# Optimization experiments

Hardware: AMD Instinct MI355X
Metric: run time of the kernel (lower is better)

Reference implementation:

```python
import jax, jax.numpy as jnp
import numpy as np

H = 16          # num_attention_heads
D = 64          # attention_head_size
HID = H * D     # hidden_size
FF = 4096       # intermediate_size
W = 128         # attention_half_width
EPS = 1e-8


def setup_inputs() -> dict:
    key = jax.random.key(0)
    ks = jax.random.split(key, 16)
    s = 0.02
    return {
        "hidden_states": jax.random.normal(ks[0], (1, 2048, HID), jnp.float32),
        "attention_mask": jnp.ones((1, 2048), dtype=bool),
        # projections stored as [in, out] (transposed torch Linear weight)
        "wq": jax.random.normal(ks[1], (HID, HID), jnp.float32) * s,
        "wk": jax.random.normal(ks[2], (HID, HID), jnp.float32) * s,
        "wv": jax.random.normal(ks[3], (HID, HID), jnp.float32) * s,
        "pos_key": jax.random.normal(ks[4], (H, D, 2 * W + 1), jnp.float32),
        "pos_query": jax.random.normal(ks[5], (H, D, 2 * W + 1), jnp.float32),
        "wo": jax.random.normal(ks[6], (HID, HID), jnp.float32) * s,
        "bo": jnp.zeros((HID,), jnp.float32),
        "ln1_g": jnp.ones((HID,), jnp.float32),
        "ln1_b": jnp.zeros((HID,), jnp.float32),
        "ln2_g": jnp.ones((HID,), jnp.float32),
        "ln2_b": jnp.zeros((HID,), jnp.float32),
        "w1": jax.random.normal(ks[7], (HID, FF), jnp.float32) * s,
        "b1": jnp.zeros((FF,), jnp.float32),
        "w2": jax.random.normal(ks[8], (FF, HID), jnp.float32) * s,
        "b2": jnp.zeros((HID,), jnp.float32),
    }


def _layer_norm(x, g, b):
    mu = jnp.mean(x, axis=-1, keepdims=True)
    var = jnp.mean(jnp.square(x - mu), axis=-1, keepdims=True)
    return (x - mu) * jax.lax.rsqrt(var + EPS) * g + b


def _encoder_layer(hidden_states, attention_mask, wq, wk, wv, pos_key,
                   pos_query, wo, bo, ln1_g, ln1_b, ln2_g, ln2_b, w1, b1, w2, b2):
    B, L, _ = hidden_states.shape
    m = attention_mask  # [B, L] bool

    # --- local self-attention with disentangled relative bias ---
    x1 = _layer_norm(hidden_states, ln1_g, ln1_b)
    q = (x1 @ wq).reshape(B, L, H, D).transpose(0, 2, 1, 3)  # [B,H,L,D]
    k = (x1 @ wk).reshape(B, L, H, D).transpose(0, 2, 1, 3)
    v = (x1 @ wv).reshape(B, L, H, D).transpose(0, 2, 1, 3)

    score = jnp.einsum('bhqd,bhkd->bhqk', q, k)  # [B,H,L,L]

    # relative position index: idx[i,j] = clip(w - (i-j), 0, 2w)
    ids = jnp.arange(L)
    idx = jnp.clip(W - (ids[:, None] - ids[None, :]), 0, 2 * W)  # [L,L]
    idx_b = jnp.broadcast_to(idx[None, None], (B, H, L, L))

    c2p = jnp.einsum('bhld,hdp->bhlp', q, pos_key)     # [B,H,L,2w+1]
    score_c2p = jnp.take_along_axis(c2p, idx_b, axis=-1)
    p2c = jnp.einsum('bhld,hdp->bhlp', k, pos_query)
    score_p2c = jnp.take_along_axis(p2c, idx_b, axis=-1).swapaxes(-1, -2)
    score = score + score_c2p + score_p2c

    band = jnp.abs(ids[:, None] - ids[None, :]) <= W   # [L,L]
    em = band[None, None] & m[:, None, None, :] & m[:, None, :, None]
    lv = jnp.finfo(score.dtype).min
    score = jnp.where(em, score, lv)
    proba = jax.nn.softmax(score, axis=-1)

    ctx = jnp.einsum('bhqk,bhkd->bhqd', proba, v)
    ctx = ctx.transpose(0, 2, 1, 3).reshape(B, L, HID)
    attn_out = ctx @ wo + bo
    h = hidden_states + attn_out  # NoGating residual

    # --- feedforward ---
    x2 = _layer_norm(h, ln2_g, ln2_b)
    ff = jax.nn.gelu(x2 @ w1 + b1, approximate=False) @ w2 + b2
    return h + ff


def reference(hidden_states, attention_mask, wq, wk, wv, pos_key, pos_query,
              wo, bo, ln1_g, ln1_b, ln2_g, ln2_b, w1, b1, w2, b2):
    return _encoder_layer(hidden_states, attention_mask, wq, wk, wv, pos_key,
                          pos_query, wo, bo, ln1_g, ln1_b, ln2_g, ln2_b,
                          w1, b1, w2, b2)
```

## Files before the change

kernel.cpp:

```cpp
#include <hip/hip_runtime.h>
#include <hip/hip_bf16.h>
#include <cstdint>

typedef __hip_bfloat16 bf16;
typedef __attribute__((ext_vector_type(8))) short short8;
typedef __attribute__((ext_vector_type(4))) float f32x4;
typedef __attribute__((address_space(1))) const unsigned int gu32;
typedef __attribute__((address_space(3))) unsigned int lu32;

#define L_SEQ 2048
#define HID_  1024
#define NH    16
#define HD    64
#define FF_   4096
#define NPOS  257
#define WHALF 128
#define QKVS  3072
#define NTILE 32
#define BT_TILE (320 * 64)

__device__ inline float b2f(bf16 v) { return __bfloat162float(v); }
__device__ inline short f2bs(float f) {
    bf16 b = __float2bfloat16(f);
    return *reinterpret_cast<short*>(&b);
}

__global__ __launch_bounds__(256) void k_transpose_tiled(const float* __restrict__ src,
                                                         bf16* __restrict__ dst,
                                                         int K, int N) {
    const int k0 = blockIdx.x * 64, n0 = blockIdx.y * 64;
    __shared__ float t[64][65];
    const int c = threadIdx.x & 63, r4 = threadIdx.x >> 6;
    #pragma unroll
    for (int i = 0; i < 16; ++i)
        t[i * 4 + r4][c] = src[(size_t)(k0 + i * 4 + r4) * N + n0 + c];
    __syncthreads();
    #pragma unroll
    for (int i = 0; i < 16; ++i) {
        int n = i * 4 + r4;
        dst[(size_t)(n0 + n) * K + k0 + c] = __float2bfloat16(t[c][n]);
    }
}

__global__ void k_pos_transpose(const float* __restrict__ src, bf16* __restrict__ dst) {
    const int total = NH * NPOS * HD;
    for (int idx = blockIdx.x * blockDim.x + threadIdx.x; idx < total;
         idx += gridDim.x * blockDim.x) {
        int d = idx & 63;
        int r = idx >> 6;
        int t = r % NPOS;
        int h = r / NPOS;
        dst[idx] = __float2bfloat16(src[((size_t)h * HD + d) * NPOS + t]);
    }
}

__global__ __launch_bounds__(256) void k_layernorm(const float* __restrict__ x,
                                                   const float* __restrict__ g,
                                                   const float* __restrict__ b,
                                                   bf16* __restrict__ out) {
    const int row = blockIdx.x, tid = threadIdx.x;
    const int lane = tid & 63, w = tid >> 6;
    const float4 v = *(const float4*)(x + (size_t)row * HID_ + tid * 4);
    float vals[4] = {v.x, v.y, v.z, v.w};
    float s = vals[0] + vals[1] + vals[2] + vals[3];
    float ss = vals[0]*vals[0] + vals[1]*vals[1] + vals[2]*vals[2] + vals[3]*vals[3];
    for (int off = 32; off; off >>= 1) { s += __shfl_down(s, off); ss += __shfl_down(ss, off); }
    __shared__ float rs[4], rss[4], mv[2];
    if (lane == 0) { rs[w] = s; rss[w] = ss; }
    __syncthreads();
    if (tid == 0) {
        float S = rs[0] + rs[1] + rs[2] + rs[3];
        float SS = rss[0] + rss[1] + rss[2] + rss[3];
        float mean = S * (1.0f / HID_);
        float var = SS * (1.0f / HID_) - mean * mean;
        mv[0] = mean; mv[1] = rsqrtf(var + 1e-8f);
    }
    __syncthreads();
    const float mean = mv[0], rstd = mv[1];
    #pragma unroll
    for (int e = 0; e < 4; ++e) {
        int c = tid * 4 + e;
        out[(size_t)row * HID_ + c] = __float2bfloat16((vals[e] - mean) * rstd * g[c] + b[c]);
    }
}

template <int EPI>
__global__ __launch_bounds__(256) void k_gemm64(const bf16* __restrict__ A,
                                                const bf16* __restrict__ B,
                                                bf16* __restrict__ outB,
                                                float* __restrict__ outF,
                                                const float* __restrict__ bias,
                                                int N, int K, int kTiles, int MN) {
    __shared__ __align__(16) short As[2][2048];
    __shared__ __align__(16) short Bs[2][4096];
    const int tid = threadIdx.x;
    const int bm = blockIdx.x * 64, bn = blockIdx.y * 128;
    const int lane = tid & 63, w = tid >> 6;
    const int wr = w >> 1, wc = w & 1;
    const int k0base = blockIdx.z * kTiles * 32;

    const int crow = lane >> 2;
    const int c16p = lane & 3;
    const int coll = (c16p ^ (crow & 3)) * 8;
    const short* Ag = (const short*)A;
    const short* Bg = (const short*)B;
    const size_t a_off = (size_t)(bm + w * 16 + crow) * K + coll;
    const size_t b_off0 = (size_t)(bn + w * 32 + crow) * K + coll;
    const size_t b_off1 = (size_t)(bn + w * 32 + 16 + crow) * K + coll;

    auto stage = [&](int buf, int k0) {
        __builtin_amdgcn_global_load_lds((gu32*)(Ag + a_off + k0), (lu32*)&As[buf][w * 512], 16, 0, 0);
        __builtin_amdgcn_global_load_lds((gu32*)(Bg + b_off0 + k0), (lu32*)&Bs[buf][w * 1024], 16, 0, 0);
        __builtin_amdgcn_global_load_lds((gu32*)(Bg + b_off1 + k0), (lu32*)&Bs[buf][w * 1024 + 512], 16, 0, 0);
    };

    const int fr = lane & 15, kq = lane >> 4;
    const int xbyte = ((kq ^ (fr & 3)) << 4);

    f32x4 acc[2][4] = {};
    stage(0, k0base);
    __syncthreads();

    for (int t = 0; t < kTiles; ++t) {
        if (t + 1 < kTiles) stage((t + 1) & 1, k0base + (t + 1) * 32);
        const char* Ab = (const char*)As[t & 1];
        const char* Bb = (const char*)Bs[t & 1];
        short8 af[2], bfv[4];
        #pragma unroll
        for (int m2 = 0; m2 < 2; ++m2)
            af[m2] = *(const short8*)(Ab + ((wr * 32 + m2 * 16 + fr) << 6) + xbyte);
        #pragma unroll
        for (int n2 = 0; n2 < 4; ++n2)
            bfv[n2] = *(const short8*)(Bb + ((wc * 64 + n2 * 16 + fr) << 6) + xbyte);
        #pragma unroll
        for (int m2 = 0; m2 < 2; ++m2)
            #pragma unroll
            for (int n2 = 0; n2 < 4; ++n2)
                acc[m2][n2] = __builtin_amdgcn_mfma_f32_16x16x32_bf16(af[m2], bfv[n2], acc[m2][n2], 0, 0, 0);
        __syncthreads();
    }

    const int cr = kq * 4, cc = fr;
    #pragma unroll
    for (int m2 = 0; m2 < 2; ++m2) {
        #pragma unroll
        for (int n2 = 0; n2 < 4; ++n2) {
            const int col = bn + wc * 64 + n2 * 16 + cc;
            #pragma unroll
            for (int e = 0; e < 4; ++e) {
                const int row = bm + wr * 32 + m2 * 16 + cr + e;
                const size_t o = (size_t)row * N + col;
                float v = acc[m2][n2][e];
                if (EPI == 0) {
                    outB[o] = __float2bfloat16(v);
                } else if (EPI == 2) {
                    float xg = v + bias[col];
                    float gl = 0.5f * xg * (1.0f + erff(xg * 0.70710678f));
                    outB[o] = __float2bfloat16(gl);
                } else {
                    outF[(size_t)blockIdx.z * MN + o] = v;
                }
            }
        }
    }
}

template <int S>
__global__ __launch_bounds__(256) void k_reduce(const float* __restrict__ parts,
                                                const float* __restrict__ bias,
                                                const float* __restrict__ res,
                                                float* __restrict__ out) {
    const int idx = blockIdx.x * 256 + threadIdx.x;
    const float4* p = (const float4*)parts;
    float4 s = p[idx];
    #pragma unroll
    for (int ss = 1; ss < S; ++ss) {
        float4 t2 = p[idx + (size_t)ss * 524288];
        s.x += t2.x; s.y += t2.y; s.z += t2.z; s.w += t2.w;
    }
    float4 bb = ((const float4*)bias)[idx & 255];
    float4 rr = ((const float4*)res)[idx];
    float4 o = {s.x + bb.x + rr.x, s.y + bb.y + rr.y, s.z + bb.z + rr.z, s.w + bb.w + rr.w};
    ((float4*)out)[idx] = o;
}

template <int MODE>
__global__ __launch_bounds__(256) void k_relpos_bt(const bf16* __restrict__ X,
                                                   const bf16* __restrict__ Pt,
                                                   bf16* __restrict__ bt) {
    const int bq = blockIdx.x, h = blockIdx.y;
    const int r0 = bq * 64;
    const int tid = threadIdx.x, lane = tid & 63, w = tid >> 6;
    const int fr = lane & 15, kg = (lane >> 4) << 3;
    const int cr = (lane >> 4) << 2, cc = lane & 15;

    short8 af[2];
    #pragma unroll
    for (int ks = 0; ks < 2; ++ks)
        af[ks] = *(const short8*)&X[(size_t)(r0 + w * 16 + fr) * QKVS + h * HD + ks * 32 + kg];

    f32x4 acc[20];
    #pragma unroll
    for (int fj = 0; fj < 20; ++fj) acc[fj] = (f32x4){0.f, 0.f, 0.f, 0.f};

    #pragma unroll
    for (int fj = 0; fj < 20; ++fj) {
        int p = fj * 16 + fr;
        int pc = p < NPOS ? p : (NPOS - 1);
        #pragma unroll
        for (int ks = 0; ks < 2; ++ks) {
            short8 bp = *(const short8*)&Pt[((size_t)h * NPOS + pc) * HD + ks * 32 + kg];
            acc[fj] = __builtin_amdgcn_mfma_f32_16x16x32_bf16(af[ks], bp, acc[fj], 0, 0, 0);
        }
    }

    #pragma unroll
    for (int fj = 0; fj < 20; ++fj) {
        int p = fj * 16 + cc;
        if (p < NPOS) {
            #pragma unroll
            for (int e = 0; e < 4; ++e) {
                int rloc = w * 16 + cr + e;
                if (MODE == 0) {
                    int t = p + rloc;
                    bt[((size_t)(h * NTILE + bq) * 320 + t) * 64 + rloc] =
                        __float2bfloat16(acc[fj][e]);
                } else {
                    int j = r0 + rloc;
                    int s = j + p - 128;
                    if (s >= 0 && s < L_SEQ) {
                        int tb = s >> 6, il = s & 63;
                        int t = j - tb * 64 + 128;
                        bt[((size_t)(h * NTILE + tb) * 320 + t) * 64 + il] =
                            __float2bfloat16(acc[fj][e]);
                    }
                }
            }
        }
    }
}

__global__ __launch_bounds__(256, 3) void k_attn_mfma(const bf16* __restrict__ qb,
                                                      const bf16* __restrict__ kb,
                                                      const bf16* __restrict__ vb,
                                                      const bf16* __restrict__ bt1,
                                                      const bf16* __restrict__ bt2,
                                                      bf16* __restrict__ ctxb) {
    const int bq = blockIdx.x, h = blockIdx.y;
    const int qi0 = bq * 64, j0 = qi0 - WHALF;
    const int tid = threadIdx.x, lane = tid & 63, w = tid >> 6;
    const int fr = lane & 15, kq = lane >> 4, kg = kq << 3;
    const int cr = kq << 2, cc = fr;

    __shared__ short KVs[20480];
    __shared__ __align__(16) short Ps[64][72];
    char* KVb = (char*)KVs;

    #pragma unroll
    for (int p = 0; p < 10; ++p) {
        int c = tid + p * 256;
        int t = c >> 3, d8 = (c & 7) << 3;
        int j = j0 + t;
        short8 v = {};
        if (j >= 0 && j < L_SEQ) v = *(const short8*)&kb[(size_t)j * QKVS + h * HD + d8];
        int byte = (t * 128 + d8 * 2) ^ ((t & 7) << 4);
        *(short8*)(KVb + byte) = v;
    }
    short8 aq[2];
    #pragma unroll
    for (int ks = 0; ks < 2; ++ks)
        aq[ks] = *(const short8*)&qb[(size_t)(qi0 + w * 16 + fr) * QKVS + h * HD + ks * 32 + kg];

    short8 ifrag = {};
    {
        int d = fr - kg;
        if (d >= 0 && d < 8) ifrag[d] = (short)0x3F80;
    }
    __syncthreads();

    f32x4 acc[20];
    #pragma unroll
    for (int fj = 0; fj < 20; ++fj) acc[fj] = (f32x4){0.f, 0.f, 0.f, 0.f};
    #pragma unroll
    for (int ks = 0; ks < 2; ++ks) {
        #pragma unroll
        for (int fj = 0; fj < 20; ++fj) {
            int t = fj * 16 + fr;
            int byte = (t * 128 + (ks * 32 + kg) * 2) ^ ((t & 7) << 4);
            short8 bk = *(const short8*)(KVb + byte);
            acc[fj] = __builtin_amdgcn_mfma_f32_16x16x32_bf16(aq[ks], bk, acc[fj], 0, 0, 0);
        }
    }
    __syncthreads();

    short8 vreg[10];
    #pragma unroll
    for (int p = 0; p < 10; ++p) {
        int c = tid + p * 256;
        int t = c >> 3, d8 = (c & 7) << 3;
        int j = j0 + t;
        short8 v = {};
        if (j >= 0 && j < L_SEQ) v = *(const short8*)&vb[(size_t)j * QKVS + h * HD + d8];
        vreg[p] = v;
    }

    {
        const short* t1 = (const short*)bt1 + (size_t)(h * NTILE + bq) * BT_TILE;
        const short* t2 = (const short*)bt2 + (size_t)(h * NTILE + bq) * BT_TILE;
        #pragma unroll
        for (int fj = 0; fj < 20; ++fj) {
            int off = (fj * 16 + fr) * 64 + w * 16 + kg;
            short8 b1 = *(const short8*)(t1 + off);
            short8 b2 = *(const short8*)(t2 + off);
            acc[fj] = __builtin_amdgcn_mfma_f32_16x16x32_bf16(ifrag, b1, acc[fj], 0, 0, 0);
            acc[fj] = __builtin_amdgcn_mfma_f32_16x16x32_bf16(ifrag, b2, acc[fj], 0, 0, 0);
        }
    }

    const int qrel0 = w * 16 + cr;
    #pragma unroll
    for (int fj = 0; fj < 20; ++fj) {
        int t = fj * 16 + cc;
        int j = j0 + t;
        #pragma unroll
        for (int e = 0; e < 4; ++e) {
            int qr = qrel0 + e;
            bool valid = (j >= 0) && (j < L_SEQ) && (t >= qr) && (t <= qr + 256);
            acc[fj][e] = valid ? acc[fj][e] : -3.0e38f;
        }
    }

    float mx[4], sm[4];
    #pragma unroll
    for (int e = 0; e < 4; ++e) {
        float m = acc[0][e];
        #pragma unroll
        for (int fj = 1; fj < 20; ++fj) m = fmaxf(m, acc[fj][e]);
        mx[e] = m;
    }
    #pragma unroll
    for (int msk = 1; msk < 16; msk <<= 1)
        #pragma unroll
        for (int e = 0; e < 4; ++e) mx[e] = fmaxf(mx[e], __shfl_xor(mx[e], msk));
    #pragma unroll
    for (int e = 0; e < 4; ++e) sm[e] = 0.f;
    #pragma unroll
    for (int fj = 0; fj < 20; ++fj)
        #pragma unroll
        for (int e = 0; e < 4; ++e) {
            float p = __expf(acc[fj][e] - mx[e]);
            acc[fj][e] = p;
            sm[e] += p;
        }
    #pragma unroll
    for (int msk = 1; msk < 16; msk <<= 1)
        #pragma unroll
        for (int e = 0; e < 4; ++e) sm[e] += __shfl_xor(sm[e], msk);
    float rinv[4];
    #pragma unroll
    for (int e = 0; e < 4; ++e) rinv[e] = 1.0f / sm[e];

    #pragma unroll
    for (int p = 0; p < 10; ++p) {
        int c = tid + p * 256;
        int t = c >> 3, d8 = (c & 7) << 3;
        #pragma unroll
        for (int e = 0; e < 8; ++e) {
            int d = d8 + e;
            int byte = (d * 640 + t * 2) ^ ((d & 7) << 4);
            *(short*)(KVb + byte) = vreg[p][e];
        }
    }

    f32x4 acc2[4];
    #pragma unroll
    for (int f = 0; f < 4; ++f) acc2[f] = (f32x4){0.f, 0.f, 0.f, 0.f};
    #pragma unroll
    for (int ch = 0; ch < 5; ++ch) {
        #pragma unroll
        for (int fjl = 0; fjl < 4; ++fjl) {
            int fj = ch * 4 + fjl;
            int col = fjl * 16 + cc;
            #pragma unroll
            for (int e = 0; e < 4; ++e)
                Ps[w * 16 + cr + e][col] = f2bs(acc[fj][e]);
        }
        if (ch == 0) __syncthreads();
        #pragma unroll
        for (int ks2 = 0; ks2 < 2; ++ks2) {
            short8 pa = *(const short8*)&Ps[w * 16 + fr][ks2 * 32 + kg];
            #pragma unroll
            for (int f = 0; f < 4; ++f) {
                int d = f * 16 + fr;
                int tg = ch * 64 + ks2 * 32 + kg;
                int byte = (d * 640 + tg * 2) ^ ((d & 7) << 4);
                short8 bv = *(const short8*)(KVb + byte);
                acc2[f] = __builtin_amdgcn_mfma_f32_16x16x32_bf16(pa, bv, acc2[f], 0, 0, 0);
            }
        }
    }

    #pragma unroll
    for (int f = 0; f < 4; ++f)
        #pragma unroll
        for (int e = 0; e < 4; ++e) {
            int row = qi0 + w * 16 + cr + e;
            int d = f * 16 + cc;
            ctxb[(size_t)row * HID_ + h * HD + d] = __float2bfloat16(acc2[f][e] * rinv[e]);
        }
}

extern "C" void kernel_launch(void* const* d_in, const int* in_sizes, int n_in,
                              void* d_out, int out_size, void* d_ws, size_t ws_size,
                              hipStream_t stream) {
    const float* hid  = (const float*)d_in[0];
    const float* wq   = (const float*)d_in[2];
    const float* wk   = (const float*)d_in[3];
    const float* wv   = (const float*)d_in[4];
    const float* pk   = (const float*)d_in[5];
    const float* pq   = (const float*)d_in[6];
    const float* wo   = (const float*)d_in[7];
    const float* bo   = (const float*)d_in[8];
    const float* ln1g = (const float*)d_in[9];
    const float* ln1b = (const float*)d_in[10];
    const float* ln2g = (const float*)d_in[11];
    const float* ln2b = (const float*)d_in[12];
    const float* w1   = (const float*)d_in[13];
    const float* b1   = (const float*)d_in[14];
    const float* w2   = (const float*)d_in[15];
    const float* b2   = (const float*)d_in[16];
    float* out = (float*)d_out;

    char* ws = (char*)d_ws;
    size_t off = 0;
    auto alloc = [&](size_t bytes) -> void* {
        void* p = ws + off;
        off += (bytes + 255) & ~(size_t)255;
        return p;
    };
    const size_t BT_BYTES = (size_t)NH * NTILE * BT_TILE * 2 + 256;
    bf16* wqkvb = (bf16*)alloc((size_t)QKVS * HID_ * 2);
    bf16* wob   = (bf16*)alloc((size_t)HID_ * HID_ * 2);
    bf16* w1b   = (bf16*)alloc((size_t)HID_ * FF_ * 2);
    bf16* w2b   = (bf16*)alloc((size_t)HID_ * FF_ * 2);
    bf16* pkt   = (bf16*)alloc((size_t)NH * NPOS * HD * 2);
    bf16* pqt   = (bf16*)alloc((size_t)NH * NPOS * HD * 2);
    bf16* x1b   = (bf16*)alloc((size_t)L_SEQ * HID_ * 2);
    bf16* qkv   = (bf16*)alloc((size_t)L_SEQ * QKVS * 2);
    bf16* bt1   = (bf16*)alloc(BT_BYTES);
    bf16* bt2   = (bf16*)alloc(BT_BYTES);
    bf16* ctxb  = (bf16*)alloc((size_t)L_SEQ * HID_ * 2);
    float* hbuf = (float*)alloc((size_t)L_SEQ * HID_ * 4);
    bf16* x2b   = (bf16*)alloc((size_t)L_SEQ * HID_ * 2);
    bf16* ffb   = (bf16*)alloc((size_t)L_SEQ * FF_ * 2);
    (void)ws_size; (void)in_sizes; (void)n_in; (void)out_size;

    float* wopart  = (float*)ffb;
    float* ff2part = (float*)qkv;

    k_transpose_tiled<<<dim3(16, 16), 256, 0, stream>>>(wq, wqkvb, 1024, 1024);
    k_transpose_tiled<<<dim3(16, 16), 256, 0, stream>>>(wk, wqkvb + (size_t)1024 * 1024, 1024, 1024);
    k_transpose_tiled<<<dim3(16, 16), 256, 0, stream>>>(wv, wqkvb + (size_t)2048 * 1024, 1024, 1024);
    k_transpose_tiled<<<dim3(16, 16), 256, 0, stream>>>(wo, wob, 1024, 1024);
    k_transpose_tiled<<<dim3(16, 64), 256, 0, stream>>>(w1, w1b, 1024, 4096);
    k_transpose_tiled<<<dim3(64, 16), 256, 0, stream>>>(w2, w2b, 4096, 1024);
    k_pos_transpose<<<1028, 256, 0, stream>>>(pk, pkt);
    k_pos_transpose<<<1028, 256, 0, stream>>>(pq, pqt);

    k_layernorm<<<L_SEQ, 256, 0, stream>>>(hid, ln1g, ln1b, x1b);

    const int MN = L_SEQ * HID_;
    k_gemm64<0><<<dim3(32, 24, 1), 256, 0, stream>>>(x1b, wqkvb, qkv, nullptr, nullptr, QKVS, HID_, 32, MN);

    dim3 g_rp(NTILE, NH);
    k_relpos_bt<0><<<g_rp, 256, 0, stream>>>(qkv, pkt, bt1);
    k_relpos_bt<1><<<g_rp, 256, 0, stream>>>(qkv + 1024, pqt, bt2);

    k_attn_mfma<<<dim3(NTILE, NH), 256, 0, stream>>>(qkv, qkv + 1024, qkv + 2048, bt1, bt2, ctxb);

    k_gemm64<3><<<dim3(32, 8, 2), 256, 0, stream>>>(ctxb, wob, nullptr, wopart, nullptr, HID_, HID_, 16, MN);
    k_reduce<2><<<2048, 256, 0, stream>>>(wopart, bo, hid, hbuf);

    k_layernorm<<<L_SEQ, 256, 0, stream>>>(hbuf, ln2g, ln2b, x2b);

    k_gemm64<2><<<dim3(32, 32, 1), 256, 0, stream>>>(x2b, w1b, ffb, nullptr, b1, FF_, HID_, 32, MN);

    k_gemm64<3><<<dim3(32, 8, 4), 256, 0, stream>>>(ffb, w2b, nullptr, ff2part, nullptr, HID_, FF_, 32, MN);
    k_reduce<4><<<2048, 256, 0, stream>>>(ff2part, b2, hbuf, out);
}
```

Measured before the change: 339.9 us.

## Enlarge GEMM tiles, fuse reduce with layernorm, batch weight prep, coalesce relpos stores

The GEMM tile grows from 64x128 to 128x128 with a 4x4 MFMA accumulator per wave and an adjusted LDS swizzle, raising operand reuse per load. The split-K reduce after the output projection is fused with the second layernorm. The six weight transposes and two pos transposes are merged into two launches. The MODE 0 relative-position bias scatter is staged through shared memory and written as coalesced 16-byte rows. In exchange there are fewer GEMM blocks, which may lower occupancy and wave count for the smaller GEMMs, and more registers per thread.

Result: faster. 327.0 us (-3.8%).

```diff
diff --git a/kernel.cpp b/kernel.cpp
--- a/kernel.cpp
+++ b/kernel.cpp
@@ -19,16 +19,32 @@
 #define NTILE 32
 #define BT_TILE (320 * 64)
 
-__device__ inline float b2f(bf16 v) { return __bfloat162float(v); }
 __device__ inline short f2bs(float f) {
     bf16 b = __float2bfloat16(f);
     return *reinterpret_cast<short*>(&b);
 }
 
-__global__ __launch_bounds__(256) void k_transpose_tiled(const float* __restrict__ src,
-                                                         bf16* __restrict__ dst,
-                                                         int K, int N) {
-    const int k0 = blockIdx.x * 64, n0 = blockIdx.y * 64;
+__global__ __launch_bounds__(256) void k_wt_all(const float* __restrict__ wq,
+                                                const float* __restrict__ wk,
+                                                const float* __restrict__ wv,
+                                                const float* __restrict__ wo,
+                                                const float* __restrict__ w1,
+                                                const float* __restrict__ w2,
+                                                bf16* __restrict__ wqkvb,
+                                                bf16* __restrict__ wob,
+                                                bf16* __restrict__ w1b,
+                                                bf16* __restrict__ w2b) {
+    const int id = blockIdx.x;
+    const float* src; bf16* dst; int K, N, tile;
+    if (id < 768)       { int s = id >> 8; tile = id & 255;
+                          src = s == 0 ? wq : (s == 1 ? wk : wv);
+                          dst = wqkvb + (size_t)s * 1024 * 1024; K = 1024; N = 1024; }
+    else if (id < 1024) { tile = id - 768;  src = wo; dst = wob; K = 1024; N = 1024; }
+    else if (id < 2048) { tile = id - 1024; src = w1; dst = w1b; K = 1024; N = 4096; }
+    else                { tile = id - 2048; src = w2; dst = w2b; K = 4096; N = 1024; }
+    const int ktiles = K >> 6;
+    const int k0 = (tile % ktiles) * 64, n0 = (tile / ktiles) * 64;
+
     __shared__ float t[64][65];
     const int c = threadIdx.x & 63, r4 = threadIdx.x >> 6;
     #pragma unroll
@@ -42,10 +58,14 @@
     }
 }
 
-__global__ void k_pos_transpose(const float* __restrict__ src, bf16* __restrict__ dst) {
-    const int total = NH * NPOS * HD;
-    for (int idx = blockIdx.x * blockDim.x + threadIdx.x; idx < total;
-         idx += gridDim.x * blockDim.x) {
+__global__ void k_pos2(const float* __restrict__ pk, const float* __restrict__ pq,
+                       bf16* __restrict__ pkt, bf16* __restrict__ pqt) {
+    const int T = NH * NPOS * HD;
+    for (int gi = blockIdx.x * blockDim.x + threadIdx.x; gi < 2 * T;
+         gi += gridDim.x * blockDim.x) {
+        const float* src = gi < T ? pk : pq;
+        bf16* dst = gi < T ? pkt : pqt;
+        int idx = gi < T ? gi : gi - T;
         int d = idx & 63;
         int r = idx >> 6;
         int t = r % NPOS;
@@ -85,39 +105,41 @@
 }
 
 template <int EPI>
-__global__ __launch_bounds__(256) void k_gemm64(const bf16* __restrict__ A,
-                                                const bf16* __restrict__ B,
-                                                bf16* __restrict__ outB,
-                                                float* __restrict__ outF,
-                                                const float* __restrict__ bias,
-                                                int N, int K, int kTiles, int MN) {
-    __shared__ __align__(16) short As[2][2048];
+__global__ __launch_bounds__(256) void k_gemm128(const bf16* __restrict__ A,
+                                                 const bf16* __restrict__ B,
+                                                 bf16* __restrict__ outB,
+                                                 float* __restrict__ outF,
+                                                 const float* __restrict__ bias,
+                                                 int N, int K, int kTiles, int MN) {
+    __shared__ __align__(16) short As[2][4096];
     __shared__ __align__(16) short Bs[2][4096];
     const int tid = threadIdx.x;
-    const int bm = blockIdx.x * 64, bn = blockIdx.y * 128;
+    const int bm = blockIdx.x * 128, bn = blockIdx.y * 128;
     const int lane = tid & 63, w = tid >> 6;
     const int wr = w >> 1, wc = w & 1;
     const int k0base = blockIdx.z * kTiles * 32;
 
     const int crow = lane >> 2;
     const int c16p = lane & 3;
-    const int coll = (c16p ^ (crow & 3)) * 8;
+    const int coll = (c16p ^ ((crow >> 1) & 3)) * 8;
     const short* Ag = (const short*)A;
     const short* Bg = (const short*)B;
-    const size_t a_off = (size_t)(bm + w * 16 + crow) * K + coll;
+    const size_t a_off0 = (size_t)(bm + w * 32 + crow) * K + coll;
+    const size_t a_off1 = (size_t)(bm + w * 32 + 16 + crow) * K + coll;
     const size_t b_off0 = (size_t)(bn + w * 32 + crow) * K + coll;
     const size_t b_off1 = (size_t)(bn + w * 32 + 16 + crow) * K + coll;
 
     auto stage = [&](int buf, int k0) {
-        __builtin_amdgcn_global_load_lds((gu32*)(Ag + a_off + k0), (lu32*)&As[buf][w * 512], 16, 0, 0);
+        __builtin_amdgcn_global_load_lds((gu32*)(Ag + a_off0 + k0), (lu32*)&As[buf][w * 1024], 16, 0, 0);
+        __builtin_amdgcn_global_load_lds((gu32*)(Ag + a_off1 + k0), (lu32*)&As[buf][w * 1024 + 512], 16, 0, 0);
         __builtin_amdgcn_global_load_lds((gu32*)(Bg + b_off0 + k0), (lu32*)&Bs[buf][w * 1024], 16, 0, 0);
         __builtin_amdgcn_global_load_lds((gu32*)(Bg + b_off1 + k0), (lu32*)&Bs[buf][w * 1024 + 512], 16, 0, 0);
     };
 
     const int fr = lane & 15, kq = lane >> 4;
-    const int xbyte = ((kq ^ (fr & 3)) << 4);
-
-    f32x4 acc[2][4] = {};
+    const int xbyte = ((kq ^ ((fr >> 1) & 3)) << 4);
+
+    f32x4 acc[4][4] = {};
     stage(0, k0base);
     __syncthreads();
 
@@ -125,15 +147,15 @@
         if (t + 1 < kTiles) stage((t + 1) & 1, k0base + (t + 1) * 32);
         const char* Ab = (const char*)As[t & 1];
         const char* Bb = (const char*)Bs[t & 1];
-        short8 af[2], bfv[4];
-        #pragma unroll
-        for (int m2 = 0; m2 < 2; ++m2)
-            af[m2] = *(const short8*)(Ab + ((wr * 32 + m2 * 16 + fr) << 6) + xbyte);
+        short8 af[4], bfv[4];
+        #pragma unroll
+        for (int m2 = 0; m2 < 4; ++m2)
+            af[m2] = *(const short8*)(Ab + ((wr * 64 + m2 * 16 + fr) << 6) + xbyte);
         #pragma unroll
         for (int n2 = 0; n2 < 4; ++n2)
             bfv[n2] = *(const short8*)(Bb + ((wc * 64 + n2 * 16 + fr) << 6) + xbyte);
         #pragma unroll
-        for (int m2 = 0; m2 < 2; ++m2)
+        for (int m2 = 0; m2 < 4; ++m2)
             #pragma unroll
             for (int n2 = 0; n2 < 4; ++n2)
                 acc[m2][n2] = __builtin_amdgcn_mfma_f32_16x16x32_bf16(af[m2], bfv[n2], acc[m2][n2], 0, 0, 0);
@@ -142,13 +164,13 @@
 
     const int cr = kq * 4, cc = fr;
     #pragma unroll
-    for (int m2 = 0; m2 < 2; ++m2) {
+    for (int m2 = 0; m2 < 4; ++m2) {
         #pragma unroll
         for (int n2 = 0; n2 < 4; ++n2) {
             const int col = bn + wc * 64 + n2 * 16 + cc;
             #pragma unroll
             for (int e = 0; e < 4; ++e) {
-                const int row = bm + wr * 32 + m2 * 16 + cr + e;
+                const int row = bm + wr * 64 + m2 * 16 + cr + e;
                 const size_t o = (size_t)row * N + col;
                 float v = acc[m2][n2][e];
                 if (EPI == 0) {
@@ -166,6 +188,51 @@
 }
 
 template <int S>
+__global__ __launch_bounds__(256) void k_reduce_ln(const float* __restrict__ parts,
+                                                   const float* __restrict__ bias,
+                                                   const float* __restrict__ res,
+                                                   const float* __restrict__ g,
+                                                   const float* __restrict__ b,
+                                                   float* __restrict__ outH,
+                                                   bf16* __restrict__ outX) {
+    const int row = blockIdx.x, tid = threadIdx.x;
+    const int lane = tid & 63, w = tid >> 6;
+    const int idx = row * 256 + tid;
+    const float4* p = (const float4*)parts;
+    float4 s = p[idx];
+    #pragma unroll
+    for (int ss = 1; ss < S; ++ss) {
+        float4 t2 = p[idx + (size_t)ss * 524288];
+        s.x += t2.x; s.y += t2.y; s.z += t2.z; s.w += t2.w;
+    }
+    float4 bb = ((const float4*)bias)[tid];
+    float4 rr = ((const float4*)res)[idx];
+    float vals[4] = {s.x + bb.x + rr.x, s.y + bb.y + rr.y, s.z + bb.z + rr.z, s.w + bb.w + rr.w};
+    ((float4*)outH)[idx] = (float4){vals[0], vals[1], vals[2], vals[3]};
+
+    float sum = vals[0] + vals[1] + vals[2] + vals[3];
+    float ssq = vals[0]*vals[0] + vals[1]*vals[1] + vals[2]*vals[2] + vals[3]*vals[3];
+    for (int off = 32; off; off >>= 1) { sum += __shfl_down(sum, off); ssq += __shfl_down(ssq, off); }
+    __shared__ float rs[4], rss[4], mv[2];
+    if (lane == 0) { rs[w] = sum; rss[w] = ssq; }
+    __syncthreads();
+    if (tid == 0) {
+        float S2 = rs[0] + rs[1] + rs[2] + rs[3];
+        float SS = rss[0] + rss[1] + rss[2] + rss[3];
+        float mean = S2 * (1.0f / HID_);
+        float var = SS * (1.0f / HID_) - mean * mean;
+        mv[0] = mean; mv[1] = rsqrtf(var + 1e-8f);
+    }
+    __syncthreads();
+    const float mean = mv[0], rstd = mv[1];
+    #pragma unroll
+    for (int e = 0; e < 4; ++e) {
+        int c = tid * 4 + e;
+        outX[(size_t)row * HID_ + c] = __float2bfloat16((vals[e] - mean) * rstd * g[c] + b[c]);
+    }
+}
+
+template <int S>
 __global__ __launch_bounds__(256) void k_reduce(const float* __restrict__ parts,
                                                 const float* __restrict__ bias,
                                                 const float* __restrict__ res,
@@ -214,18 +281,39 @@
         }
     }
 
-    #pragma unroll
-    for (int fj = 0; fj < 20; ++fj) {
-        int p = fj * 16 + cc;
-        if (p < NPOS) {
+    if (MODE == 0) {
+        __shared__ short ld[64][328];
+        #pragma unroll
+        for (int fj = 0; fj < 20; ++fj) {
+            int p = fj * 16 + cc;
+            if (p < NPOS) {
+                #pragma unroll
+                for (int e = 0; e < 4; ++e)
+                    ld[w * 16 + cr + e][p] = f2bs(acc[fj][e]);
+            }
+        }
+        __syncthreads();
+        short* outp = (short*)bt + (size_t)(h * NTILE + bq) * BT_TILE;
+        #pragma unroll
+        for (int i = 0; i < 10; ++i) {
+            int idx8 = (tid + i * 256) * 8;
+            int t = idx8 >> 6, il0 = idx8 & 63;
+            short8 v;
             #pragma unroll
-            for (int e = 0; e < 4; ++e) {
-                int rloc = w * 16 + cr + e;
-                if (MODE == 0) {
-                    int t = p + rloc;
-                    bt[((size_t)(h * NTILE + bq) * 320 + t) * 64 + rloc] =
-                        __float2bfloat16(acc[fj][e]);
-                } else {
+            for (int e = 0; e < 8; ++e) {
+                int il = il0 + e, p = t - il;
+                v[e] = (p >= 0 && p < NPOS) ? ld[il][p] : (short)0;
+            }
+            *(short8*)(outp + t * 64 + il0) = v;
+        }
+    } else {
+        #pragma unroll
+        for (int fj = 0; fj < 20; ++fj) {
+            int p = fj * 16 + cc;
+            if (p < NPOS) {
+                #pragma unroll
+                for (int e = 0; e < 4; ++e) {
+                    int rloc = w * 16 + cr + e;
                     int j = r0 + rloc;
                     int s = j + p - 128;
                     if (s >= 0 && s < L_SEQ) {
@@ -458,19 +546,13 @@
     float* wopart  = (float*)ffb;
     float* ff2part = (float*)qkv;
 
-    k_transpose_tiled<<<dim3(16, 16), 256, 0, stream>>>(wq, wqkvb, 1024, 1024);
-    k_transpose_tiled<<<dim3(16, 16), 256, 0, stream>>>(wk, wqkvb + (size_t)1024 * 1024, 1024, 1024);
-    k_transpose_tiled<<<dim3(16, 16), 256, 0, stream>>>(wv, wqkvb + (size_t)2048 * 1024, 1024, 1024);
-    k_transpose_tiled<<<dim3(16, 16), 256, 0, stream>>>(wo, wob, 1024, 1024);
-    k_transpose_tiled<<<dim3(16, 64), 256, 0, stream>>>(w1, w1b, 1024, 4096);
-    k_transpose_tiled<<<dim3(64, 16), 256, 0, stream>>>(w2, w2b, 4096, 1024);
-    k_pos_transpose<<<1028, 256, 0, stream>>>(pk, pkt);
-    k_pos_transpose<<<1028, 256, 0, stream>>>(pq, pqt);
+    k_wt_all<<<3072, 256, 0, stream>>>(wq, wk, wv, wo, w1, w2, wqkvb, wob, w1b, w2b);
+    k_pos2<<<2056, 256, 0, stream>>>(pk, pq, pkt, pqt);
 
     k_layernorm<<<L_SEQ, 256, 0, stream>>>(hid, ln1g, ln1b, x1b);
 
     const int MN = L_SEQ * HID_;
-    k_gemm64<0><<<dim3(32, 24, 1), 256, 0, stream>>>(x1b, wqkvb, qkv, nullptr, nullptr, QKVS, HID_, 32, MN);
+    k_gemm128<0><<<dim3(16, 24, 1), 256, 0, stream>>>(x1b, wqkvb, qkv, nullptr, nullptr, QKVS, HID_, 32, MN);
 
     dim3 g_rp(NTILE, NH);
     k_relpos_bt<0><<<g_rp, 256, 0, stream>>>(qkv, pkt, bt1);
@@ -478,13 +560,11 @@
 
     k_attn_mfma<<<dim3(NTILE, NH), 256, 0, stream>>>(qkv, qkv + 1024, qkv + 2048, bt1, bt2, ctxb);
 
-    k_gemm64<3><<<dim3(32, 8, 2), 256, 0, stream>>>(ctxb, wob, nullptr, wopart, nullptr, HID_, HID_, 16, MN);
-    k_reduce<2><<<2048, 256, 0, stream>>>(wopart, bo, hid, hbuf);
-
-    k_layernorm<<<L_SEQ, 256, 0, stream>>>(hbuf, ln2g, ln2b, x2b);
-
-    k_gemm64<2><<<dim3(32, 32, 1), 256, 0, stream>>>(x2b, w1b, ffb, nullptr, b1, FF_, HID_, 32, MN);
-
-    k_gemm64<3><<<dim3(32, 8, 4), 256, 0, stream>>>(ffb, w2b, nullptr, ff2part, nullptr, HID_, FF_, 32, MN);
+    k_gemm128<3><<<dim3(16, 8, 2), 256, 0, stream>>>(ctxb, wob, nullptr, wopart, nullptr, HID_, HID_, 16, MN);
+    k_reduce_ln<2><<<L_SEQ, 256, 0, stream>>>(wopart, bo, hid, ln2g, ln2b, hbuf, x2b);
+
+    k_gemm128<2><<<dim3(16, 32, 1), 256, 0, stream>>>(x2b, w1b, ffb, nullptr, b1, FF_, HID_, 32, MN);
+
+    k_gemm128<3><<<dim3(16, 8, 4), 256, 0, stream>>>(ffb, w2b, nullptr, ff2part, nullptr, HID_, FF_, 32, MN);
     k_reduce<4><<<2048, 256, 0, stream>>>(ff2part, b2, hbuf, out);
 }
```
